# Kernel optimization log

Hardware: AMD Instinct MI355X
Metric: run time of the kernel (lower is better)

## Reference

```python
import jax, jax.numpy as jnp
import numpy as np

N = 100000   # nodes
E = 1600000  # edges (avg degree 16)
H = 128      # hidden
S = 10000    # subgraphs
G = 64       # graphs


def setup_inputs() -> dict:
    key = jax.random.key(0)
    ks = jax.random.split(key, 8)
    def w(k, shape, fan_in):
        return jax.random.normal(k, shape, dtype=jnp.float32) * (1.0 / np.sqrt(fan_in))
    return {
        "x": jnp.ones((N, 1), dtype=jnp.float32),
        "edge_index": jax.random.randint(ks[0], (2, E), 0, N, dtype=jnp.int64),
        "node_to_subgraph": jnp.sort(jax.random.randint(ks[1], (N,), 0, S, dtype=jnp.int64)),
        "subgraph_to_graph": jnp.sort(jax.random.randint(ks[2], (S,), 0, G, dtype=jnp.int64)),
        "conv1_W1": w(ks[3], (1, H), 1),
        "conv1_b1": jnp.zeros((H,), jnp.float32),
        "conv1_W2": w(ks[4], (H, H), H),
        "conv1_b2": jnp.zeros((H,), jnp.float32),
        "convs_W1": w(ks[5], (2, H, H), H),
        "convs_b1": jnp.zeros((2, H), jnp.float32),
        "convs_W2": w(ks[6], (2, H, H), H),
        "convs_b2": jnp.zeros((2, H), jnp.float32),
    }


def _gin_layer(x, src, dst, W1, b1, W2, b2):
    # GINConv, train_eps=False, eps=0: nn((1+0)*x + sum_{j in N(i)} x_j)
    agg = jax.ops.segment_sum(x[src], dst, num_segments=x.shape[0])
    h = jax.nn.relu((x + agg) @ W1 + b1)
    return jax.nn.relu(h @ W2 + b2)


def reference(x, edge_index, node_to_subgraph, subgraph_to_graph,
              conv1_W1, conv1_b1, conv1_W2, conv1_b2,
              convs_W1, convs_b1, convs_W2, convs_b2):
    src, dst = edge_index[0], edge_index[1]
    h = _gin_layer(x, src, dst, conv1_W1, conv1_b1, conv1_W2, conv1_b2)
    for i in range(convs_W1.shape[0]):  # num_layers - 1 = 2 structurally distinct layers
        h = _gin_layer(h, src, dst, convs_W1[i], convs_b1[i], convs_W2[i], convs_b2[i])
    # global_add_pool over node_to_subgraph, then subgraph_to_graph
    h = jax.ops.segment_sum(h, node_to_subgraph, num_segments=S)
    h = jax.ops.segment_sum(h, subgraph_to_graph, num_segments=G)
    return h  # [G, H]
```

## Files before the change

kernel.cpp:

```cpp
#include <hip/hip_runtime.h>

typedef unsigned int u32;
typedef unsigned short u16;
typedef __attribute__((ext_vector_type(8))) short bf16x8;
typedef __attribute__((ext_vector_type(4))) float f32x4;

#define CAP 2560
#define CHUNK 8192
#define GMT 2

__device__ __forceinline__ float bfl(u32 v){ return __uint_as_float(v << 16); }
__device__ __forceinline__ float bfh(u32 v){ return __uint_as_float(v & 0xffff0000u); }
__device__ __forceinline__ u16 f2bf(float f){
    u32 u = __float_as_uint(f);
    u += 0x7fffu + ((u >> 16) & 1u);
    return (u16)(u >> 16);
}
__device__ __forceinline__ u32 pack2(float a, float b){
    u32 ua = __float_as_uint(a); ua += 0x7fffu + ((ua >> 16) & 1u);
    u32 ub = __float_as_uint(b); ub += 0x7fffu + ((ub >> 16) & 1u);
    return (ua >> 16) | (ub & 0xffff0000u);
}


__global__ __launch_bounds__(256) void bucket_count(const int* __restrict__ dst,
                                                    const int* __restrict__ src,
                                                    int* __restrict__ gcur,
                                                    u32* __restrict__ slots,
                                                    int NBk, int E){
    __shared__ int cnt[800];
    int t = threadIdx.x;
    int e0 = blockIdx.x * CHUNK;
    for (int i = t; i < NBk; i += 256) cnt[i] = 0;
    __syncthreads();
    #pragma unroll
    for (int k = 0; k < CHUNK / 256; k++){
        int e = e0 + t + k * 256;
        if (e < E) atomicAdd(&cnt[dst[e] >> 7], 1);
    }
    __syncthreads();
    for (int i = t; i < NBk; i += 256){
        int c = cnt[i];
        cnt[i] = c ? atomicAdd(&gcur[i], c) : 0;
    }
    __syncthreads();
    #pragma unroll
    for (int k = 0; k < CHUNK / 256; k++){
        int e = e0 + t + k * 256;
        if (e < E){
            int d = dst[e];
            int b = d >> 7;
            int pos = atomicAdd(&cnt[b], 1);
            if (pos < CAP) slots[b * CAP + pos] = ((u32)(d & 127) << 17) | (u32)src[e];
        }
    }
}


__global__ __launch_bounds__(256) void bucket_csr(const int* __restrict__ gcur,
                                                  u32* __restrict__ csr,
                                                  int* __restrict__ starts,
                                                  int* __restrict__ ends,
                                                  const float* __restrict__ x,
                                                  const int* __restrict__ n2s,
                                                  const int* __restrict__ s2g,
                                                  float* __restrict__ sval,
                                                  int* __restrict__ gmap, int N){
    __shared__ u32 ebuf[CAP];
    __shared__ int cnt[128], excl[128], cur[128];
    __shared__ float sacc[128];
    int b = blockIdx.x, t = threadIdx.x;
    int base = b * CAP;
    int sz = gcur[b]; if (sz > CAP) sz = CAP;
    if (t < 128){ cnt[t] = 0; sacc[t] = 0.f; }
    __syncthreads();
    for (int i = t; i < sz; i += 256){
        u32 p = csr[base + i];
        ebuf[i] = p;
        atomicAdd(&cnt[p >> 17], 1);
        atomicAdd(&sacc[p >> 17], x[p & 0x1FFFFu]);
    }
    __syncthreads();
    if (t < 64){
        int c0 = cnt[2 * t], c1 = cnt[2 * t + 1];
        int tot = c0 + c1;
        int incl = tot;
        #pragma unroll
        for (int o = 1; o < 64; o <<= 1){
            int v = __shfl_up(incl, o);
            if (t >= o) incl += v;
        }
        int ex = incl - tot;
        excl[2 * t] = ex;
        excl[2 * t + 1] = ex + c0;
    }
    __syncthreads();
    if (t < 128){
        int node = b * 128 + t;
        if (node < N){
            int st = base + excl[t];
            starts[node] = st;
            ends[node] = st + cnt[t];
            sval[node] = x[node] + sacc[t];
            gmap[node] = s2g[n2s[node]];
        }
        cur[t] = excl[t];
    }
    __syncthreads();
    for (int i = t; i < sz; i += 256){
        u32 p = ebuf[i];
        int dl = p >> 17;
        int r = atomicAdd(&cur[dl], 1);
        csr[base + r] = p & 0x1FFFFu;
    }
}


struct W5 { const float* p[5]; };

__global__ void pack_k(W5 w5, u16* __restrict__ wp,
                       int* __restrict__ gcur, int ngcur,
                       float* __restrict__ outz, int nout){
    int m = blockIdx.x;
    int t = threadIdx.x;
    if (m == 5){
        for (int i = t; i < ngcur; i += 256) gcur[i] = 0;
        return;
    }
    if (m == 6){
        for (int i = t; i < nout; i += 256) outz[i] = 0.f;
        return;
    }
    const float* W = w5.p[m];
    u16* dstp = wp + m * 16384;
    #pragma unroll
    for (int it = 0; it < 8; it++){
        int task = t + 256 * it;
        int n = task & 127, c = task >> 7;
        u16 tmp[8];
        #pragma unroll
        for (int j = 0; j < 8; j++) tmp[j] = f2bf(W[(c * 8 + j) * 128 + n]);
        uint4 val;
        val.x = (u32)tmp[0] | ((u32)tmp[1] << 16);
        val.y = (u32)tmp[2] | ((u32)tmp[3] << 16);
        val.z = (u32)tmp[4] | ((u32)tmp[5] << 16);
        val.w = (u32)tmp[6] | ((u32)tmp[7] << 16);
        *(uint4*)(dstp + n * 128 + ((c ^ ((n >> 3) & 15)) << 3)) = val;
    }
}


__global__ __launch_bounds__(256) void gemm1_fused(const float* __restrict__ sval,
                                                   const float* __restrict__ W1,
                                                   const float* __restrict__ b1,
                                                   const u16* __restrict__ Wp,
                                                   const float* __restrict__ bias,
                                                   u16* __restrict__ Out, int nrows){
    __shared__ uint4 ldsbuf[2048];
    __shared__ float w1s[128], b1s[128];
    u16* lds = (u16*)ldsbuf;
    int t = threadIdx.x;
    const uint4* wsrc = (const uint4*)Wp;
    #pragma unroll
    for (int j = 0; j < 8; j++) ldsbuf[t + 256 * j] = wsrc[t + 256 * j];
    if (t < 128){ w1s[t] = W1[t]; b1s[t] = b1[t]; }
    __syncthreads();

    int wave = t >> 6, lane = t & 63;
    int m = lane & 15, q = lane >> 4;
    int r0 = blockIdx.x * (64 * GMT) + wave * (16 * GMT);

    float sv[GMT];
    #pragma unroll
    for (int mt = 0; mt < GMT; mt++){
        int row = r0 + mt * 16 + m;
        if (row >= nrows) row = nrows - 1;
        sv[mt] = sval[row];
    }

    f32x4 acc[GMT][8];
    #pragma unroll
    for (int a = 0; a < GMT; a++)
        #pragma unroll
        for (int b = 0; b < 8; b++){ f32x4 z = {0.f, 0.f, 0.f, 0.f}; acc[a][b] = z; }

    #pragma unroll
    for (int kt = 0; kt < 4; kt++){
        int c = kt * 4 + q;
        int k0 = kt * 32 + q * 8;
        float wk[8], bk[8];
        #pragma unroll
        for (int j = 0; j < 8; j++){ wk[j] = w1s[k0 + j]; bk[j] = b1s[k0 + j]; }
        bf16x8 bfrag[8];
        #pragma unroll
        for (int nt = 0; nt < 8; nt++){
            int n = m * 8 + nt;
            bfrag[nt] = *(const bf16x8*)(lds + n * 128 + ((c ^ m) << 3));
        }
        #pragma unroll
        for (int mt = 0; mt < GMT; mt++){
            bf16x8 afrag;
            #pragma unroll
            for (int j = 0; j < 8; j++){
                float v = sv[mt] * wk[j] + bk[j];
                v = v > 0.f ? v : 0.f;
                afrag[j] = (short)f2bf(v);
            }
            #pragma unroll
            for (int nt = 0; nt < 8; nt++)
                acc[mt][nt] = __builtin_amdgcn_mfma_f32_16x16x32_bf16(afrag, bfrag[nt], acc[mt][nt], 0, 0, 0);
        }
    }

    float4 bb0 = *(const float4*)(bias + m * 8);
    float4 bb1 = *(const float4*)(bias + m * 8 + 4);
    float bb[8] = {bb0.x, bb0.y, bb0.z, bb0.w, bb1.x, bb1.y, bb1.z, bb1.w};
    #pragma unroll
    for (int mt = 0; mt < GMT; mt++){
        #pragma unroll
        for (int r = 0; r < 4; r++){
            int row = r0 + mt * 16 + q * 4 + r;
            if (row < nrows){
                float v[8];
                #pragma unroll
                for (int j = 0; j < 8; j++){
                    float vv = acc[mt][j][r] + bb[j];
                    v[j] = vv > 0.f ? vv : 0.f;
                }
                uint4 o;
                o.x = pack2(v[0], v[1]);
                o.y = pack2(v[2], v[3]);
                o.z = pack2(v[4], v[5]);
                o.w = pack2(v[6], v[7]);
                *(uint4*)(Out + row * 128 + m * 8) = o;
            }
        }
    }
}


__global__ __launch_bounds__(256) void gemm2_fused(const u16* A,
                                                   const u16* __restrict__ Wp1,
                                                   const u16* __restrict__ Wp2,
                                                   const float* __restrict__ bias1,
                                                   const float* __restrict__ bias2,
                                                   u16* Out, int nrows){
    __shared__ uint4 buf1[2048];
    __shared__ uint4 buf2[2048];
    u16* lds1 = (u16*)buf1;
    u16* lds2 = (u16*)buf2;
    int t = threadIdx.x;
    #pragma unroll
    for (int j = 0; j < 8; j++){
        buf1[t + 256 * j] = ((const uint4*)Wp1)[t + 256 * j];
        buf2[t + 256 * j] = ((const uint4*)Wp2)[t + 256 * j];
    }
    __syncthreads();

    int wave = t >> 6, lane = t & 63;
    int m = lane & 15, q = lane >> 4;
    int rl0 = wave * (16 * GMT);
    int r0 = blockIdx.x * (64 * GMT) + rl0;

    f32x4 acc[GMT][8];
    #pragma unroll
    for (int a = 0; a < GMT; a++)
        #pragma unroll
        for (int b = 0; b < 8; b++){ f32x4 z = {0.f, 0.f, 0.f, 0.f}; acc[a][b] = z; }

    #pragma unroll
    for (int kt = 0; kt < 4; kt++){
        int c = kt * 4 + q;
        bf16x8 bfrag[8];
        #pragma unroll
        for (int nt = 0; nt < 8; nt++){
            int n = m * 8 + nt;
            bfrag[nt] = *(const bf16x8*)(lds1 + n * 128 + ((c ^ m) << 3));
        }
        #pragma unroll
        for (int mt = 0; mt < GMT; mt++){
            int row = r0 + mt * 16 + m;
            if (row >= nrows) row = nrows - 1;
            bf16x8 afrag = *(const bf16x8*)(A + row * 128 + kt * 32 + q * 8);
            #pragma unroll
            for (int nt = 0; nt < 8; nt++)
                acc[mt][nt] = __builtin_amdgcn_mfma_f32_16x16x32_bf16(afrag, bfrag[nt], acc[mt][nt], 0, 0, 0);
        }
    }
    __syncthreads();

    {
        float4 bb0 = *(const float4*)(bias1 + m * 8);
        float4 bb1 = *(const float4*)(bias1 + m * 8 + 4);
        float bb[8] = {bb0.x, bb0.y, bb0.z, bb0.w, bb1.x, bb1.y, bb1.z, bb1.w};
        #pragma unroll
        for (int mt = 0; mt < GMT; mt++){
            #pragma unroll
            for (int r = 0; r < 4; r++){
                int rl = rl0 + mt * 16 + q * 4 + r;
                float v[8];
                #pragma unroll
                for (int j = 0; j < 8; j++){
                    float vv = acc[mt][j][r] + bb[j];
                    v[j] = vv > 0.f ? vv : 0.f;
                }
                uint4 o;
                o.x = pack2(v[0], v[1]);
                o.y = pack2(v[2], v[3]);
                o.z = pack2(v[4], v[5]);
                o.w = pack2(v[6], v[7]);
                *(uint4*)(lds1 + rl * 128 + ((m ^ (rl & 15)) << 3)) = o;
            }
        }
    }
    __syncthreads();

    #pragma unroll
    for (int a = 0; a < GMT; a++)
        #pragma unroll
        for (int b = 0; b < 8; b++){ f32x4 z = {0.f, 0.f, 0.f, 0.f}; acc[a][b] = z; }

    #pragma unroll
    for (int kt = 0; kt < 4; kt++){
        int c = kt * 4 + q;
        bf16x8 bfrag[8];
        #pragma unroll
        for (int nt = 0; nt < 8; nt++){
            int n = m * 8 + nt;
            bfrag[nt] = *(const bf16x8*)(lds2 + n * 128 + ((c ^ m) << 3));
        }
        #pragma unroll
        for (int mt = 0; mt < GMT; mt++){
            int rl = rl0 + mt * 16 + m;
            bf16x8 afrag = *(const bf16x8*)(lds1 + rl * 128 + (((kt * 4 + q) ^ (rl & 15)) << 3));
            #pragma unroll
            for (int nt = 0; nt < 8; nt++)
                acc[mt][nt] = __builtin_amdgcn_mfma_f32_16x16x32_bf16(afrag, bfrag[nt], acc[mt][nt], 0, 0, 0);
        }
    }

    float4 bb0 = *(const float4*)(bias2 + m * 8);
    float4 bb1 = *(const float4*)(bias2 + m * 8 + 4);
    float bb[8] = {bb0.x, bb0.y, bb0.z, bb0.w, bb1.x, bb1.y, bb1.z, bb1.w};
    #pragma unroll
    for (int mt = 0; mt < GMT; mt++){
        #pragma unroll
        for (int r = 0; r < 4; r++){
            int row = r0 + mt * 16 + q * 4 + r;
            if (row < nrows){
                float v[8];
                #pragma unroll
                for (int j = 0; j < 8; j++){
                    float vv = acc[mt][j][r] + bb[j];
                    v[j] = vv > 0.f ? vv : 0.f;
                }
                uint4 o;
                o.x = pack2(v[0], v[1]);
                o.y = pack2(v[2], v[3]);
                o.z = pack2(v[4], v[5]);
                o.w = pack2(v[6], v[7]);
                *(uint4*)(Out + row * 128 + m * 8) = o;
            }
        }
    }
}


__device__ __forceinline__ void acc8(float* a, uint4 u){
    a[0] += bfl(u.x); a[1] += bfh(u.x);
    a[2] += bfl(u.y); a[3] += bfh(u.y);
    a[4] += bfl(u.z); a[5] += bfh(u.z);
    a[6] += bfl(u.w); a[7] += bfh(u.w);
}

__global__ __launch_bounds__(256) void agg_k(const uint4* __restrict__ Hin, uint4* __restrict__ Hout,
                                             const int* __restrict__ starts, const int* __restrict__ ends,
                                             const u32* __restrict__ csr, int N){
    int gtid = blockIdx.x * 256 + threadIdx.x;
    int node = gtid >> 4;
    int c = threadIdx.x & 15;
    if (node >= N) return;

    uint4 v = Hin[node * 16 + c];
    float a[8];
    a[0] = bfl(v.x); a[1] = bfh(v.x);
    a[2] = bfl(v.y); a[3] = bfh(v.y);
    a[4] = bfl(v.z); a[5] = bfh(v.z);
    a[6] = bfl(v.w); a[7] = bfh(v.w);

    int b0 = starts[node], b1 = ends[node];
    int j = b0;
    for (; j + 4 <= b1; j += 4){
        int s0 = csr[j], s1 = csr[j + 1], s2 = csr[j + 2], s3 = csr[j + 3];
        uint4 u0 = Hin[s0 * 16 + c];
        uint4 u1 = Hin[s1 * 16 + c];
        uint4 u2 = Hin[s2 * 16 + c];
        uint4 u3 = Hin[s3 * 16 + c];
        acc8(a, u0); acc8(a, u1); acc8(a, u2); acc8(a, u3);
    }
    for (; j < b1; j++){
        int s = csr[j];
        uint4 u = Hin[s * 16 + c];
        acc8(a, u);
    }

    uint4 o;
    o.x = pack2(a[0], a[1]);
    o.y = pack2(a[2], a[3]);
    o.z = pack2(a[4], a[5]);
    o.w = pack2(a[6], a[7]);
    Hout[node * 16 + c] = o;
}


__global__ __launch_bounds__(256) void pool2_k(const u32* __restrict__ H,
                                               const int* __restrict__ gmap,
                                               float* __restrict__ out, int N){
    int c = threadIdx.x & 63;
    int seg = blockIdx.x * 4 + (threadIdx.x >> 6);
    int start = seg * 64;
    if (start >= N) return;
    int end = start + 64; if (end > N) end = N;
    int g = gmap[start];
    float a0 = 0.f, a1 = 0.f;
    for (int n = start; n < end; n++){
        int gn = gmap[n];
        if (gn != g){
            unsafeAtomicAdd(&out[g * 128 + 2 * c], a0);
            unsafeAtomicAdd(&out[g * 128 + 2 * c + 1], a1);
            a0 = 0.f; a1 = 0.f; g = gn;
        }
        u32 u = H[n * 64 + c];
        a0 += bfl(u);
        a1 += bfh(u);
    }
    unsafeAtomicAdd(&out[g * 128 + 2 * c], a0);
    unsafeAtomicAdd(&out[g * 128 + 2 * c + 1], a1);
}

extern "C" void kernel_launch(void* const* d_in, const int* in_sizes, int n_in,
                              void* d_out, int out_size, void* d_ws, size_t ws_size,
                              hipStream_t stream){
    const float* x    = (const float*)d_in[0];
    const int*   ei   = (const int*)d_in[1];
    const int*   n2s  = (const int*)d_in[2];
    const int*   s2g  = (const int*)d_in[3];
    const float* c1W1 = (const float*)d_in[4];
    const float* c1b1 = (const float*)d_in[5];
    const float* c1W2 = (const float*)d_in[6];
    const float* c1b2 = (const float*)d_in[7];
    const float* cW1  = (const float*)d_in[8];
    const float* cb1  = (const float*)d_in[9];
    const float* cW2  = (const float*)d_in[10];
    const float* cb2  = (const float*)d_in[11];
    float* out = (float*)d_out;

    int N = in_sizes[0];
    int E = in_sizes[1] / 2;
    const int* src = ei;
    const int* dst = ei + E;
    int NBk = (N + 127) / 128;

    char* w = (char*)d_ws;
    size_t off = 0;
    auto al = [&](size_t b){ size_t r = off; off += (b + 255) & ~(size_t)255; return r; };
    int*   gcur   = (int*)(w + al((size_t)NBk * 4));
    int*   starts = (int*)(w + al((size_t)N * 4));
    int*   ends   = (int*)(w + al((size_t)N * 4));
    float* sval   = (float*)(w + al((size_t)N * 4));
    int*   gmap   = (int*)(w + al((size_t)N * 4));
    u32*   csr    = (u32*)(w + al((size_t)NBk * CAP * 4));
    u16*   wp     = (u16*)(w + al((size_t)5 * 16384 * 2));
    u16*   P      = (u16*)(w + al((size_t)N * 128 * 2));
    u16*   Q      = (u16*)(w + al((size_t)N * 128 * 2));

    W5 w5;
    w5.p[0] = c1W2;
    w5.p[1] = cW1;
    w5.p[2] = cW2;
    w5.p[3] = cW1 + 16384;
    w5.p[4] = cW2 + 16384;
    pack_k<<<7, 256, 0, stream>>>(w5, wp, gcur, NBk, out, out_size);

    bucket_count<<<(E + CHUNK - 1) / CHUNK, 256, 0, stream>>>(dst, src, gcur, csr, NBk, E);
    bucket_csr<<<NBk, 256, 0, stream>>>(gcur, csr, starts, ends, x, n2s, s2g, sval, gmap, N);

    int gG = (N + 64 * GMT - 1) / (64 * GMT);
    int gA = (N * 16 + 255) / 256;
    gemm1_fused<<<gG, 256, 0, stream>>>(sval, c1W1, c1b1, wp + 0 * 16384, c1b2, P, N);
    agg_k<<<gA, 256, 0, stream>>>((const uint4*)P, (uint4*)Q, starts, ends, csr, N);
    gemm2_fused<<<gG, 256, 0, stream>>>(Q, wp + 1 * 16384, wp + 2 * 16384, cb1, cb2, Q, N);
    agg_k<<<gA, 256, 0, stream>>>((const uint4*)Q, (uint4*)P, starts, ends, csr, N);
    gemm2_fused<<<gG, 256, 0, stream>>>(P, wp + 3 * 16384, wp + 4 * 16384, cb1 + 128, cb2 + 128, P, N);
    pool2_k<<<(N + 255) / 256, 256, 0, stream>>>((const u32*)P, gmap, out, N);
}
```

Baseline: 336.5 us.

## Fuse neighbor aggregation into MLP GEMM kernel, read weights from global

Merges the gather-sum aggregation kernel with the two-layer MLP kernel. Each block aggregates its 128 rows straight into LDS and then runs both GEMMs from there, so the aggregated features never make a round trip through HBM and two launches are removed. Weight fragments are now read from global memory (L2/L1) instead of being staged in LDS, which halves LDS use per block. The costs are less parallelism during the gather phase, since each thread now handles 8 nodes in sequence, and uncached weight reads that could add latency.

```diff
diff --git a/kernel.cpp b/kernel.cpp
--- a/kernel.cpp
+++ b/kernel.cpp
@@ -239,28 +239,70 @@
 }
 
 
-__global__ __launch_bounds__(256) void gemm2_fused(const u16* A,
-                                                   const u16* __restrict__ Wp1,
-                                                   const u16* __restrict__ Wp2,
-                                                   const float* __restrict__ bias1,
-                                                   const float* __restrict__ bias2,
-                                                   u16* Out, int nrows){
-    __shared__ uint4 buf1[2048];
-    __shared__ uint4 buf2[2048];
-    u16* lds1 = (u16*)buf1;
-    u16* lds2 = (u16*)buf2;
+__device__ __forceinline__ void acc8(float* a, uint4 u){
+    a[0] += bfl(u.x); a[1] += bfh(u.x);
+    a[2] += bfl(u.y); a[3] += bfh(u.y);
+    a[4] += bfl(u.z); a[5] += bfh(u.z);
+    a[6] += bfl(u.w); a[7] += bfh(u.w);
+}
+
+__global__ __launch_bounds__(256) void agg_mlp_fused(const uint4* __restrict__ Hin,
+                                                     const u16* __restrict__ Wp1,
+                                                     const u16* __restrict__ Wp2,
+                                                     const float* __restrict__ bias1,
+                                                     const float* __restrict__ bias2,
+                                                     const int* __restrict__ starts,
+                                                     const int* __restrict__ ends,
+                                                     const u32* __restrict__ csr,
+                                                     u16* __restrict__ Out, int nrows){
+    __shared__ uint4 hbuf[2048];
+    u16* lds = (u16*)hbuf;
     int t = threadIdx.x;
-    #pragma unroll
-    for (int j = 0; j < 8; j++){
-        buf1[t + 256 * j] = ((const uint4*)Wp1)[t + 256 * j];
-        buf2[t + 256 * j] = ((const uint4*)Wp2)[t + 256 * j];
+    int r0blk = blockIdx.x * 128;
+
+    {
+        int gi = t >> 4;
+        int c = t & 15;
+        #pragma unroll
+        for (int it = 0; it < 8; it++){
+            int rl = it * 16 + gi;
+            int node = r0blk + rl;
+            if (node < nrows){
+                uint4 v = Hin[node * 16 + c];
+                float a[8];
+                a[0] = bfl(v.x); a[1] = bfh(v.x);
+                a[2] = bfl(v.y); a[3] = bfh(v.y);
+                a[4] = bfl(v.z); a[5] = bfh(v.z);
+                a[6] = bfl(v.w); a[7] = bfh(v.w);
+                int b0 = starts[node], b1 = ends[node];
+                int j = b0;
+                for (; j + 4 <= b1; j += 4){
+                    int s0 = csr[j], s1 = csr[j + 1], s2 = csr[j + 2], s3 = csr[j + 3];
+                    uint4 u0 = Hin[s0 * 16 + c];
+                    uint4 u1 = Hin[s1 * 16 + c];
+                    uint4 u2 = Hin[s2 * 16 + c];
+                    uint4 u3 = Hin[s3 * 16 + c];
+                    acc8(a, u0); acc8(a, u1); acc8(a, u2); acc8(a, u3);
+                }
+                for (; j < b1; j++){
+                    uint4 u = Hin[csr[j] * 16 + c];
+                    acc8(a, u);
+                }
+                uint4 o;
+                o.x = pack2(a[0], a[1]);
+                o.y = pack2(a[2], a[3]);
+                o.z = pack2(a[4], a[5]);
+                o.w = pack2(a[6], a[7]);
+                *(uint4*)(lds + rl * 128 + ((c ^ (rl & 15)) << 3)) = o;
+            }
+        }
     }
     __syncthreads();
 
     int wave = t >> 6, lane = t & 63;
     int m = lane & 15, q = lane >> 4;
     int rl0 = wave * (16 * GMT);
-    int r0 = blockIdx.x * (64 * GMT) + rl0;
+    int r0 = r0blk + rl0;
 
     f32x4 acc[GMT][8];
     #pragma unroll
@@ -275,13 +317,12 @@
         #pragma unroll
         for (int nt = 0; nt < 8; nt++){
             int n = m * 8 + nt;
-            bfrag[nt] = *(const bf16x8*)(lds1 + n * 128 + ((c ^ m) << 3));
+            bfrag[nt] = *(const bf16x8*)(Wp1 + n * 128 + ((c ^ m) << 3));
         }
         #pragma unroll
         for (int mt = 0; mt < GMT; mt++){
-            int row = r0 + mt * 16 + m;
-            if (row >= nrows) row = nrows - 1;
-            bf16x8 afrag = *(const bf16x8*)(A + row * 128 + kt * 32 + q * 8);
+            int rl = rl0 + mt * 16 + m;
+            bf16x8 afrag = *(const bf16x8*)(lds + rl * 128 + ((c ^ (rl & 15)) << 3));
             #pragma unroll
             for (int nt = 0; nt < 8; nt++)
                 acc[mt][nt] = __builtin_amdgcn_mfma_f32_16x16x32_bf16(afrag, bfrag[nt], acc[mt][nt], 0, 0, 0);
@@ -309,7 +350,7 @@
                 o.y = pack2(v[2], v[3]);
                 o.z = pack2(v[4], v[5]);
                 o.w = pack2(v[6], v[7]);
-                *(uint4*)(lds1 + rl * 128 + ((m ^ (rl & 15)) << 3)) = o;
+                *(uint4*)(lds + rl * 128 + ((m ^ (rl & 15)) << 3)) = o;
             }
         }
     }
@@ -327,12 +368,12 @@
         #pragma unroll
         for (int nt = 0; nt < 8; nt++){
             int n = m * 8 + nt;
-            bfrag[nt] = *(const bf16x8*)(lds2 + n * 128 + ((c ^ m) << 3));
+            bfrag[nt] = *(const bf16x8*)(Wp2 + n * 128 + ((c ^ m) << 3));
         }
         #pragma unroll
         for (int mt = 0; mt < GMT; mt++){
             int rl = rl0 + mt * 16 + m;
-            bf16x8 afrag = *(const bf16x8*)(lds1 + rl * 128 + (((kt * 4 + q) ^ (rl & 15)) << 3));
+            bf16x8 afrag = *(const bf16x8*)(lds + rl * 128 + ((c ^ (rl & 15)) << 3));
             #pragma unroll
             for (int nt = 0; nt < 8; nt++)
                 acc[mt][nt] = __builtin_amdgcn_mfma_f32_16x16x32_bf16(afrag, bfrag[nt], acc[mt][nt], 0, 0, 0);
@@ -366,53 +407,6 @@
 }
 
 
-__device__ __forceinline__ void acc8(float* a, uint4 u){
-    a[0] += bfl(u.x); a[1] += bfh(u.x);
-    a[2] += bfl(u.y); a[3] += bfh(u.y);
-    a[4] += bfl(u.z); a[5] += bfh(u.z);
-    a[6] += bfl(u.w); a[7] += bfh(u.w);
-}
-
-__global__ __launch_bounds__(256) void agg_k(const uint4* __restrict__ Hin, uint4* __restrict__ Hout,
-                                             const int* __restrict__ starts, const int* __restrict__ ends,
-                                             const u32* __restrict__ csr, int N){
-    int gtid = blockIdx.x * 256 + threadIdx.x;
-    int node = gtid >> 4;
-    int c = threadIdx.x & 15;
-    if (node >= N) return;
-
-    uint4 v = Hin[node * 16 + c];
-    float a[8];
-    a[0] = bfl(v.x); a[1] = bfh(v.x);
-    a[2] = bfl(v.y); a[3] = bfh(v.y);
-    a[4] = bfl(v.z); a[5] = bfh(v.z);
-    a[6] = bfl(v.w); a[7] = bfh(v.w);
-
-    int b0 = starts[node], b1 = ends[node];
-    int j = b0;
-    for (; j + 4 <= b1; j += 4){
-        int s0 = csr[j], s1 = csr[j + 1], s2 = csr[j + 2], s3 = csr[j + 3];
-        uint4 u0 = Hin[s0 * 16 + c];
-        uint4 u1 = Hin[s1 * 16 + c];
-        uint4 u2 = Hin[s2 * 16 + c];
-        uint4 u3 = Hin[s3 * 16 + c];
-        acc8(a, u0); acc8(a, u1); acc8(a, u2); acc8(a, u3);
-    }
-    for (; j < b1; j++){
-        int s = csr[j];
-        uint4 u = Hin[s * 16 + c];
-        acc8(a, u);
-    }
-
-    uint4 o;
-    o.x = pack2(a[0], a[1]);
-    o.y = pack2(a[2], a[3]);
-    o.z = pack2(a[4], a[5]);
-    o.w = pack2(a[6], a[7]);
-    Hout[node * 16 + c] = o;
-}
-
-
 __global__ __launch_bounds__(256) void pool2_k(const u32* __restrict__ H,
                                                const int* __restrict__ gmap,
                                                float* __restrict__ out, int N){
@@ -486,11 +480,10 @@
     bucket_csr<<<NBk, 256, 0, stream>>>(gcur, csr, starts, ends, x, n2s, s2g, sval, gmap, N);
 
     int gG = (N + 64 * GMT - 1) / (64 * GMT);
-    int gA = (N * 16 + 255) / 256;
     gemm1_fused<<<gG, 256, 0, stream>>>(sval, c1W1, c1b1, wp + 0 * 16384, c1b2, P, N);
-    agg_k<<<gA, 256, 0, stream>>>((const uint4*)P, (uint4*)Q, starts, ends, csr, N);
-    gemm2_fused<<<gG, 256, 0, stream>>>(Q, wp + 1 * 16384, wp + 2 * 16384, cb1, cb2, Q, N);
-    agg_k<<<gA, 256, 0, stream>>>((const uint4*)Q, (uint4*)P, starts, ends, csr, N);
-    gemm2_fused<<<gG, 256, 0, stream>>>(P, wp + 3 * 16384, wp + 4 * 16384, cb1 + 128, cb2 + 128, P, N);
+    agg_mlp_fused<<<gG, 256, 0, stream>>>((const uint4*)P, wp + 1 * 16384, wp + 2 * 16384,
+                                          cb1, cb2, starts, ends, csr, Q, N);
+    agg_mlp_fused<<<gG, 256, 0, stream>>>((const uint4*)Q, wp + 3 * 16384, wp + 4 * 16384,
+                                          cb1 + 128, cb2 + 128, starts, ends, csr, P, N);
     pool2_k<<<(N + 255) / 256, 256, 0, stream>>>((const u32*)P, gmap, out, N);
 }
```

After: 410.8 us. +22.1%, slower.
